# Kernel optimization log

Hardware: AMD Instinct MI355X
Metric: run time of the kernel (lower is better)

The kernel has to match this reference:

```python
import jax, jax.numpy as jnp
import numpy as np

B, T, D = 1, 2048, 4096
H, KV, HD = 32, 8, 128          # num_heads, num_kv_heads, head_dim
G = H // KV                     # kv groups
ROPE_THETA = 1000000.0
EPS = 1e-6


def _rmsnorm(x, w):
    # per-last-dim RMSNorm in fp32, as in Qwen3RMSNorm
    var = jnp.mean(jnp.square(x.astype(jnp.float32)), axis=-1, keepdims=True)
    return w * (x * jax.lax.rsqrt(var + EPS)).astype(x.dtype)


def _rotate_half(x):
    x1, x2 = x[..., : HD // 2], x[..., HD // 2 :]
    return jnp.concatenate([-x2, x1], axis=-1)


def setup_inputs() -> dict:
    key = jax.random.key(0)
    ks = jax.random.split(key, 7)
    s = 1.0 / np.sqrt(D)
    return {
        "hidden_states": jax.random.normal(ks[0], (B, T, D), dtype=jnp.float32),
        "Wq": jax.random.normal(ks[1], (D, H * HD), dtype=jnp.float32) * s,
        "Wk": jax.random.normal(ks[2], (D, KV * HD), dtype=jnp.float32) * s,
        "Wv": jax.random.normal(ks[3], (D, KV * HD), dtype=jnp.float32) * s,
        "Wo": jax.random.normal(ks[4], (H * HD, D), dtype=jnp.float32) * s,
        "q_norm_w": jnp.ones((HD,), dtype=jnp.float32),
        "k_norm_w": jnp.ones((HD,), dtype=jnp.float32),
    }


def reference(hidden_states, Wq, Wk, Wv, Wo, q_norm_w, k_norm_w):
    x = hidden_states
    # projections -> [B, heads, T, HD]
    q = (x @ Wq).reshape(B, T, H, HD).transpose(0, 2, 1, 3)
    k = (x @ Wk).reshape(B, T, KV, HD).transpose(0, 2, 1, 3)
    v = (x @ Wv).reshape(B, T, KV, HD).transpose(0, 2, 1, 3)

    # QK RMSNorm over head_dim
    q = _rmsnorm(q, q_norm_w)
    k = _rmsnorm(k, k_norm_w)

    # RoPE (self-attention path)
    inv_freq = 1.0 / (ROPE_THETA ** (jnp.arange(0, HD, 2, dtype=jnp.float32) / HD))
    freqs = jnp.arange(T, dtype=jnp.float32)[:, None] * inv_freq[None, :]  # [T, HD/2]
    emb = jnp.concatenate([freqs, freqs], axis=-1)                        # [T, HD]
    cos, sin = jnp.cos(emb)[None, None], jnp.sin(emb)[None, None]
    q = q * cos + _rotate_half(q) * sin
    k = k * cos + _rotate_half(k) * sin

    # GQA: group Q heads instead of repeat_interleaving K/V
    qg = q.reshape(B, KV, G, T, HD)  # head h attends kv head h // G
    scale = 1.0 / np.sqrt(HD)
    scores = jnp.einsum("bkgqd,bksd->bkgqs", qg, k) * scale  # [B,KV,G,Tq,Ts]

    causal = jnp.tril(jnp.ones((T, T), dtype=bool))
    scores = jnp.where(causal[None, None, None], scores, -jnp.inf)
    attn = jax.nn.softmax(scores, axis=-1)

    out = jnp.einsum("bkgqs,bksd->bkgqd", attn, v)            # [B,KV,G,T,HD]
    out = out.reshape(B, H, T, HD).transpose(0, 2, 1, 3).reshape(B, T, H * HD)
    return out @ Wo
```

## Files before the change

kernel.cpp:

```cpp
#include <hip/hip_runtime.h>
#include <math.h>

typedef __bf16 bf16;
typedef __bf16 bf16x8 __attribute__((ext_vector_type(8)));
typedef float f32x4 __attribute__((ext_vector_type(4)));

constexpr int cT = 2048;
constexpr int cD = 4096;
constexpr int cH = 32;
constexpr int cKV = 8;
constexpr int cHD = 128;
constexpr float SCALE = 0.08838834764831845f;

__device__ __forceinline__ void gl_lds16(const bf16* g, bf16* l) {
  __builtin_amdgcn_global_load_lds(
      (const __attribute__((address_space(1))) unsigned*)g,
      (__attribute__((address_space(3))) unsigned*)l, 16, 0, 0);
}

__device__ inline bf16x8 load8_cvt(const float* __restrict__ p) {
  float4 a = *(const float4*)p;
  float4 b = *(const float4*)(p + 4);
  bf16x8 r;
  r[0] = (bf16)a.x; r[1] = (bf16)a.y; r[2] = (bf16)a.z; r[3] = (bf16)a.w;
  r[4] = (bf16)b.x; r[5] = (bf16)b.y; r[6] = (bf16)b.z; r[7] = (bf16)b.w;
  return r;
}

__global__ __launch_bounds__(256) void convert_kernel(const float* __restrict__ s,
                                                      bf16* __restrict__ d) {
  const size_t i = (size_t)(blockIdx.x * 256 + threadIdx.x) * 8;
  *(bf16x8*)(d + i) = load8_cvt(s + i);
}

__global__ __launch_bounds__(256) void convT_kernel(const float* __restrict__ src,
                                                    bf16* __restrict__ dst,
                                                    int R, int C) {
  __shared__ float t[64][65];
  const int r0 = blockIdx.y * 64, c0 = blockIdx.x * 64;
  const int tid = threadIdx.x;
  {
    const int lr = tid >> 4, lc = (tid & 15) * 4;
#pragma unroll
    for (int i = 0; i < 4; ++i) {
      float4 v4 = *(const float4*)(src + (size_t)(r0 + lr + i * 16) * C + c0 + lc);
      t[lr + i * 16][lc] = v4.x;
      t[lr + i * 16][lc + 1] = v4.y;
      t[lr + i * 16][lc + 2] = v4.z;
      t[lr + i * 16][lc + 3] = v4.w;
    }
  }
  __syncthreads();
  {
    const int c = tid >> 2, rb = (tid & 3) * 16;
#pragma unroll
    for (int half = 0; half < 2; ++half) {
      bf16x8 o;
#pragma unroll
      for (int j = 0; j < 8; ++j) o[j] = (bf16)t[rb + half * 8 + j][c];
      *(bf16x8*)(dst + (size_t)(c0 + c) * R + r0 + rb + half * 8) = o;
    }
  }
}

template <int BN, typename OutT>
__global__ __launch_bounds__(256) void gemm_bt_kernel(const bf16* __restrict__ A,
                                                      const bf16* __restrict__ BT,
                                                      OutT* __restrict__ C,
                                                      int M, int N, int K) {
  __shared__ __align__(16) bf16 As[128][32];
  __shared__ __align__(16) bf16 Bs[BN][32];
  constexpr int TN = BN / 32;

  const int tid = threadIdx.x;
  const int lane = tid & 63, w = tid >> 6;
  const int ln = lane & 15, kg = lane >> 4;
  const int m0 = blockIdx.y * 128, n0 = blockIdx.x * BN;
  const int wm = (w >> 1) * 64;
  const int wn = (w & 1) * (BN / 2);

  f32x4 acc[4][TN] = {};

  const int srow = lane >> 2;
  const int schk = (lane & 3) * 8;
  const bf16* aG = A + (size_t)(m0 + srow) * K + schk;
  const bf16* bG = BT + (size_t)(n0 + srow) * K + schk;

  for (int kt = 0; kt < K; kt += 32) {
#pragma unroll
    for (int j = 0; j < 2; ++j)
      gl_lds16(aG + (size_t)(w * 32 + j * 16) * K + kt, &As[w * 32 + j * 16][0]);
#pragma unroll
    for (int j = 0; j < BN / 64; ++j)
      gl_lds16(bG + (size_t)(w * (BN / 4) + j * 16) * K + kt,
               &Bs[w * (BN / 4) + j * 16][0]);
    __syncthreads();

    bf16x8 af[4], bfr[TN];
#pragma unroll
    for (int tm = 0; tm < 4; ++tm)
      af[tm] = *(const bf16x8*)(&As[wm + tm * 16 + ln][kg * 8]);
#pragma unroll
    for (int tn = 0; tn < TN; ++tn)
      bfr[tn] = *(const bf16x8*)(&Bs[wn + tn * 16 + ln][kg * 8]);
#pragma unroll
    for (int tm = 0; tm < 4; ++tm)
#pragma unroll
      for (int tn = 0; tn < TN; ++tn)
        acc[tm][tn] = __builtin_amdgcn_mfma_f32_16x16x32_bf16(
            af[tm], bfr[tn], acc[tm][tn], 0, 0, 0);
    __syncthreads();
  }

#pragma unroll
  for (int tm = 0; tm < 4; ++tm)
#pragma unroll
    for (int tn = 0; tn < TN; ++tn)
#pragma unroll
      for (int r = 0; r < 4; ++r)
        C[(size_t)(m0 + wm + tm * 16 + kg * 4 + r) * N + n0 + wn + tn * 16 + ln] =
            (OutT)acc[tm][tn][r];
}

__global__ __launch_bounds__(256) void norm_rope_kernel(bf16* __restrict__ q,
                                                        bf16* __restrict__ kv,
                                                        const float* __restrict__ qw,
                                                        const float* __restrict__ kw) {
  const int gw = (blockIdx.x * 256 + threadIdx.x) >> 6;
  const int lane = threadIdx.x & 63;
  bf16* base;
  const float* wgt;
  float post;
  int t;
  if (gw < cT * cH) {
    t = gw >> 5;
    int h = gw & 31;
    base = q + (size_t)t * (cH * cHD) + h * cHD;
    wgt = qw;
    post = SCALE;
  } else {
    int g2 = gw - cT * cH;
    t = g2 >> 3;
    int h = g2 & 7;
    base = kv + (size_t)t * (2 * cKV * cHD) + h * cHD;
    wgt = kw;
    post = 1.0f;
  }
  const int d0 = lane * 2;
  float x0 = (float)base[d0], x1 = (float)base[d0 + 1];
  float ss = x0 * x0 + x1 * x1;
#pragma unroll
  for (int off = 32; off > 0; off >>= 1) ss += __shfl_xor(ss, off, 64);
  const float rs = rsqrtf(ss * (1.0f / 128.0f) + 1e-6f);
  float y0 = x0 * rs * wgt[d0];
  float y1 = x1 * rs * wgt[d0 + 1];
  float p0 = __shfl_xor(y0, 32, 64);
  float p1 = __shfl_xor(y1, 32, 64);
  const float sgn = (lane < 32) ? -1.0f : 1.0f;
  const int fi = d0 & 63;
  const float c1 = -19.93156856932417f / 64.0f;
  float inv0 = exp2f((float)fi * c1);
  float inv1 = exp2f((float)(fi + 1) * c1);
  float a0 = (float)t * inv0, a1 = (float)t * inv1;
  float o0 = (y0 * cosf(a0) + sgn * p0 * sinf(a0)) * post;
  float o1 = (y1 * cosf(a1) + sgn * p1 * sinf(a1)) * post;
  base[d0] = (bf16)o0;
  base[d0 + 1] = (bf16)o1;
}

__global__ void bound_kernel(const float* __restrict__ qw,
                             const float* __restrict__ kw,
                             float* __restrict__ cb) {
  const int lane = threadIdx.x;
  float mq = fmaxf(fabsf(qw[lane]), fabsf(qw[lane + 64]));
  float mk = fmaxf(fabsf(kw[lane]), fabsf(kw[lane + 64]));
#pragma unroll
  for (int off = 32; off > 0; off >>= 1) {
    mq = fmaxf(mq, __shfl_xor(mq, off, 64));
    mk = fmaxf(mk, __shfl_xor(mk, off, 64));
  }
  if (lane == 0) *cb = 128.0f * SCALE * mq * mk + 1e-3f;
}

__global__ __launch_bounds__(256) void flash_kernel(const bf16* __restrict__ q,
                                                    const bf16* __restrict__ kv,
                                                    const float* __restrict__ cb,
                                                    bf16* __restrict__ out) {
  __shared__ bf16 Ks[64][136];
  __shared__ bf16 VT[128][72];
  __shared__ bf16 Ps[4][32][72];

  constexpr int KVS = 2 * cKV * cHD;
  const int qt = gridDim.x - 1 - blockIdx.x;
  const int h = blockIdx.y;
  const int qm0 = qt * 128;
  const int kh = h >> 2;
  const int tid = threadIdx.x;
  const int lane = tid & 63, w = tid >> 6;
  const int ln = lane & 15, kg = lane >> 4;
  const float C = *cb;
  const int row0 = qm0 + w * 32;

  bf16x8 qa[2][4];
#pragma unroll
  for (int mt = 0; mt < 2; ++mt) {
    const bf16* qrow =
        q + (size_t)(row0 + mt * 16 + ln) * (cH * cHD) + h * cHD + kg * 8;
#pragma unroll
    for (int kk = 0; kk < 4; ++kk) qa[mt][kk] = *(const bf16x8*)(qrow + kk * 32);
  }

  const int sl = tid >> 2, sc = tid & 3;
  const int vp = tid & 31, vc = tid >> 5;

  float l_r[2][4] = {};
  f32x4 o_acc[2][8] = {};

  const int nkt = 2 * qt + 2;
  for (int kt = 0; kt < nkt; ++kt) {
    {
      const bf16* krow = kv + (size_t)(kt * 64 + sl) * KVS + kh * cHD + sc * 32;
#pragma unroll
      for (int i = 0; i < 4; ++i)
        *(bf16x8*)(&Ks[sl][sc * 32 + i * 8]) = *(const bf16x8*)(krow + i * 8);
    }
    {
      const bf16* vrow =
          kv + cKV * cHD + (size_t)(kt * 64 + 2 * vp) * KVS + kh * cHD + vc * 16;
      bf16x8 a0 = *(const bf16x8*)(vrow);
      bf16x8 a1 = *(const bf16x8*)(vrow + 8);
      bf16x8 b0 = *(const bf16x8*)(vrow + KVS);
      bf16x8 b1 = *(const bf16x8*)(vrow + KVS + 8);
#pragma unroll
      for (int i = 0; i < 8; ++i) {
        union { bf16 hh[2]; unsigned u; } pk;
        pk.hh[0] = a0[i]; pk.hh[1] = b0[i];
        *(unsigned*)(&VT[vc * 16 + i][2 * vp]) = pk.u;
        pk.hh[0] = a1[i]; pk.hh[1] = b1[i];
        *(unsigned*)(&VT[vc * 16 + 8 + i][2 * vp]) = pk.u;
      }
    }
    __syncthreads();

    f32x4 s_acc[2][4] = {};
#pragma unroll
    for (int kk = 0; kk < 4; ++kk)
#pragma unroll
      for (int nt = 0; nt < 4; ++nt) {
        bf16x8 bfr = *(const bf16x8*)(&Ks[nt * 16 + ln][kk * 32 + kg * 8]);
        s_acc[0][nt] = __builtin_amdgcn_mfma_f32_16x16x32_bf16(
            qa[0][kk], bfr, s_acc[0][nt], 0, 0, 0);
        s_acc[1][nt] = __builtin_amdgcn_mfma_f32_16x16x32_bf16(
            qa[1][kk], bfr, s_acc[1][nt], 0, 0, 0);
      }

    const bool edge = (kt * 64 + 63 > row0);
#pragma unroll
    for (int mt = 0; mt < 2; ++mt)
#pragma unroll
      for (int nt = 0; nt < 4; ++nt)
#pragma unroll
        for (int r = 0; r < 4; ++r) {
          float pe = __expf(s_acc[mt][nt][r] - C);
          if (edge) {
            int col = kt * 64 + nt * 16 + ln;
            int row = row0 + mt * 16 + kg * 4 + r;
            if (col > row) pe = 0.f;
          }
          l_r[mt][r] += pe;
          Ps[w][mt * 16 + kg * 4 + r][nt * 16 + ln] = (bf16)pe;
        }

#pragma unroll
    for (int kk2 = 0; kk2 < 2; ++kk2) {
      bf16x8 pa0 = *(const bf16x8*)(&Ps[w][ln][kk2 * 32 + kg * 8]);
      bf16x8 pa1 = *(const bf16x8*)(&Ps[w][16 + ln][kk2 * 32 + kg * 8]);
#pragma unroll
      for (int dt = 0; dt < 8; ++dt) {
        bf16x8 vb = *(const bf16x8*)(&VT[dt * 16 + ln][kk2 * 32 + kg * 8]);
        o_acc[0][dt] = __builtin_amdgcn_mfma_f32_16x16x32_bf16(
            pa0, vb, o_acc[0][dt], 0, 0, 0);
        o_acc[1][dt] = __builtin_amdgcn_mfma_f32_16x16x32_bf16(
            pa1, vb, o_acc[1][dt], 0, 0, 0);
      }
    }
    __syncthreads();
  }

#pragma unroll
  for (int mt = 0; mt < 2; ++mt)
#pragma unroll
    for (int r = 0; r < 4; ++r) {
      float l = l_r[mt][r];
#pragma unroll
      for (int off = 1; off <= 8; off <<= 1) l += __shfl_xor(l, off, 64);
      l_r[mt][r] = 1.0f / l;
    }

#pragma unroll
  for (int mt = 0; mt < 2; ++mt) {
    bf16* op = out + (size_t)(row0 + mt * 16 + kg * 4) * (cH * cHD) + h * cHD + ln;
#pragma unroll
    for (int dt = 0; dt < 8; ++dt)
#pragma unroll
      for (int r = 0; r < 4; ++r)
        op[(size_t)r * (cH * cHD) + dt * 16] = (bf16)(o_acc[mt][dt][r] * l_r[mt][r]);
  }
}

extern "C" void kernel_launch(void* const* d_in, const int* in_sizes, int n_in,
                              void* d_out, int out_size, void* d_ws, size_t ws_size,
                              hipStream_t stream) {
  const float* x  = (const float*)d_in[0];
  const float* Wq = (const float*)d_in[1];
  const float* Wk = (const float*)d_in[2];
  const float* Wv = (const float*)d_in[3];
  const float* Wo = (const float*)d_in[4];
  const float* qw = (const float*)d_in[5];
  const float* kw = (const float*)d_in[6];
  float* out = (float*)d_out;

  char* ws = (char*)d_ws;
  bf16* xb   = (bf16*)ws;
  bf16* WqT  = (bf16*)(ws + (16u << 20));
  bf16* WkvT = (bf16*)(ws + (16u << 20));
  bf16* kvb  = (bf16*)(ws + (32u << 20));
  float* cb  = (float*)(ws + (46u << 20));
  bf16* qb   = (bf16*)(ws + (48u << 20));
  bf16* attn = (bf16*)ws;
  bf16* WoT  = (bf16*)(ws + (16u << 20));

  convert_kernel<<<(cT * cD) / (8 * 256), 256, 0, stream>>>(x, xb);
  convT_kernel<<<dim3(cD / 64, cD / 64), 256, 0, stream>>>(Wq, WqT, cD, cD);
  gemm_bt_kernel<128, bf16><<<dim3(cD / 128, cT / 128), 256, 0, stream>>>(
      xb, WqT, qb, cT, cD, cD);
  convT_kernel<<<dim3((cKV * cHD) / 64, cD / 64), 256, 0, stream>>>(Wk, WkvT, cD, cKV * cHD);
  convT_kernel<<<dim3((cKV * cHD) / 64, cD / 64), 256, 0, stream>>>(
      Wv, WkvT + (size_t)(cKV * cHD) * cD, cD, cKV * cHD);
  gemm_bt_kernel<64, bf16><<<dim3((2 * cKV * cHD) / 64, cT / 128), 256, 0, stream>>>(
      xb, WkvT, kvb, cT, 2 * cKV * cHD, cD);
  norm_rope_kernel<<<(cT * (cH + cKV)) / 4, 256, 0, stream>>>(qb, kvb, qw, kw);
  bound_kernel<<<1, 64, 0, stream>>>(qw, kw, cb);
  flash_kernel<<<dim3(cT / 128, cH), 256, 0, stream>>>(qb, kvb, cb, attn);
  convT_kernel<<<dim3(cD / 64, cD / 64), 256, 0, stream>>>(Wo, WoT, cD, cD);
  gemm_bt_kernel<128, float><<<dim3(cD / 128, cT / 128), 256, 0, stream>>>(
      attn, WoT, out, cT, cD, cD);
}
```

Measured before the change: 635.1 us.

## Prefetch next K/V tile into registers, balance causal work, raise MFMA priority

The flash attention loop now loads the next K/V tile from global memory into registers while the current tile's MFMAs run, so the memory latency is hidden behind compute. The block-to-query-tile mapping is also changed so half the heads walk tiles in reverse order, which spreads the uneven causal workload across the grid. s_setprio is raised around the MFMA sections to favour matrix issue. The prefetch adds register pressure and may lower occupancy.

```diff
diff --git a/kernel.cpp b/kernel.cpp
--- a/kernel.cpp
+++ b/kernel.cpp
@@ -191,7 +191,7 @@
   __shared__ bf16 Ps[4][32][72];
 
   constexpr int KVS = 2 * cKV * cHD;
-  const int qt = gridDim.x - 1 - blockIdx.x;
+  const int qt = (blockIdx.y < 16) ? (15 - blockIdx.x) : blockIdx.x;
   const int h = blockIdx.y;
   const int qm0 = qt * 128;
   const int kh = h >> 2;
@@ -212,37 +212,49 @@
 
   const int sl = tid >> 2, sc = tid & 3;
   const int vp = tid & 31, vc = tid >> 5;
+  const bf16* kbase = kv + (size_t)sl * KVS + kh * cHD + sc * 32;
+  const bf16* vbase = kv + cKV * cHD + (size_t)(2 * vp) * KVS + kh * cHD + vc * 16;
 
   float l_r[2][4] = {};
   f32x4 o_acc[2][8] = {};
 
   const int nkt = 2 * qt + 2;
+
+  bf16x8 kr[4], vr[4];
+#pragma unroll
+  for (int i = 0; i < 4; ++i) kr[i] = *(const bf16x8*)(kbase + i * 8);
+  vr[0] = *(const bf16x8*)(vbase);
+  vr[1] = *(const bf16x8*)(vbase + 8);
+  vr[2] = *(const bf16x8*)(vbase + KVS);
+  vr[3] = *(const bf16x8*)(vbase + KVS + 8);
+
   for (int kt = 0; kt < nkt; ++kt) {
-    {
-      const bf16* krow = kv + (size_t)(kt * 64 + sl) * KVS + kh * cHD + sc * 32;
-#pragma unroll
-      for (int i = 0; i < 4; ++i)
-        *(bf16x8*)(&Ks[sl][sc * 32 + i * 8]) = *(const bf16x8*)(krow + i * 8);
-    }
-    {
-      const bf16* vrow =
-          kv + cKV * cHD + (size_t)(kt * 64 + 2 * vp) * KVS + kh * cHD + vc * 16;
-      bf16x8 a0 = *(const bf16x8*)(vrow);
-      bf16x8 a1 = *(const bf16x8*)(vrow + 8);
-      bf16x8 b0 = *(const bf16x8*)(vrow + KVS);
-      bf16x8 b1 = *(const bf16x8*)(vrow + KVS + 8);
-#pragma unroll
-      for (int i = 0; i < 8; ++i) {
-        union { bf16 hh[2]; unsigned u; } pk;
-        pk.hh[0] = a0[i]; pk.hh[1] = b0[i];
-        *(unsigned*)(&VT[vc * 16 + i][2 * vp]) = pk.u;
-        pk.hh[0] = a1[i]; pk.hh[1] = b1[i];
-        *(unsigned*)(&VT[vc * 16 + 8 + i][2 * vp]) = pk.u;
-      }
+#pragma unroll
+    for (int i = 0; i < 4; ++i)
+      *(bf16x8*)(&Ks[sl][sc * 32 + i * 8]) = kr[i];
+#pragma unroll
+    for (int i = 0; i < 8; ++i) {
+      union { bf16 hh[2]; unsigned u; } pk;
+      pk.hh[0] = vr[0][i]; pk.hh[1] = vr[2][i];
+      *(unsigned*)(&VT[vc * 16 + i][2 * vp]) = pk.u;
+      pk.hh[0] = vr[1][i]; pk.hh[1] = vr[3][i];
+      *(unsigned*)(&VT[vc * 16 + 8 + i][2 * vp]) = pk.u;
     }
     __syncthreads();
 
+    if (kt + 1 < nkt) {
+      const bf16* kn = kbase + (size_t)(kt + 1) * 64 * KVS;
+      const bf16* vn = vbase + (size_t)(kt + 1) * 64 * KVS;
+#pragma unroll
+      for (int i = 0; i < 4; ++i) kr[i] = *(const bf16x8*)(kn + i * 8);
+      vr[0] = *(const bf16x8*)(vn);
+      vr[1] = *(const bf16x8*)(vn + 8);
+      vr[2] = *(const bf16x8*)(vn + KVS);
+      vr[3] = *(const bf16x8*)(vn + KVS + 8);
+    }
+
     f32x4 s_acc[2][4] = {};
+    __builtin_amdgcn_s_setprio(1);
 #pragma unroll
     for (int kk = 0; kk < 4; ++kk)
 #pragma unroll
@@ -253,6 +265,7 @@
         s_acc[1][nt] = __builtin_amdgcn_mfma_f32_16x16x32_bf16(
             qa[1][kk], bfr, s_acc[1][nt], 0, 0, 0);
       }
+    __builtin_amdgcn_s_setprio(0);
 
     const bool edge = (kt * 64 + 63 > row0);
 #pragma unroll
@@ -271,6 +284,7 @@
           Ps[w][mt * 16 + kg * 4 + r][nt * 16 + ln] = (bf16)pe;
         }
 
+    __builtin_amdgcn_s_setprio(1);
 #pragma unroll
     for (int kk2 = 0; kk2 < 2; ++kk2) {
       bf16x8 pa0 = *(const bf16x8*)(&Ps[w][ln][kk2 * 32 + kg * 8]);
@@ -284,6 +298,7 @@
             pa1, vb, o_acc[1][dt], 0, 0, 0);
       }
     }
+    __builtin_amdgcn_s_setprio(0);
     __syncthreads();
   }
 
```

Result: faster. 595.1 us (-6.3%).
